# Performance work log

Hardware: AMD Instinct MI355X
Metric: run time of the kernel (lower is better)

The kernel has to match this reference:

```python
import jax, jax.numpy as jnp
import numpy as np
from jax import lax

N = 2048
BS = 64
NUM_ITR = 25


def setup_inputs() -> dict:
    key = jax.random.key(0)
    k1, k2, k3, k4, k5 = jax.random.split(key, 5)
    scale = 0.5 / np.sqrt(N)  # keep iteration matrices contractive so the recurrence stays bounded
    H = jax.random.normal(k1, (N, N), dtype=jnp.float32) / np.sqrt(N)
    Dinv = jax.random.normal(k2, (N, N), dtype=jnp.float32) * scale
    U = jax.random.normal(k3, (N, N), dtype=jnp.float32) * scale
    invM = jax.random.normal(k4, (N, N), dtype=jnp.float32) * scale
    y = jax.random.normal(k5, (BS, N), dtype=jnp.float32)
    return {"num_itr": NUM_ITR, "bs": BS, "y": y, "H": H, "Dinv": Dinv, "U": U, "invM": invM}


def reference(num_itr, bs, y, H, Dinv, U, invM):
    n = H.shape[0]
    s0 = jnp.zeros((bs, n), dtype=y.dtype)
    yMF = y @ H.T                 # [bs, n]
    s_init = yMF @ Dinv           # initial Gauss-Seidel estimate

    def step(s, _):
        s_next = (yMF - s @ U) @ invM
        return s_next, s_next

    s_final, traj_iters = lax.scan(step, s_init, None, length=num_itr)
    # traj matches the torch list: [zeros, s_1, ..., s_num_itr]
    traj = jnp.concatenate([s0[None], traj_iters], axis=0)  # [num_itr+1, bs, n]
    return s_final, traj
```

## Files before the change

kernel.cpp:

```cpp
#include <hip/hip_runtime.h>
#include <hip/hip_bf16.h>

#define NDIM 2048
#define BS   64
#define NM4  (NDIM * NDIM / 4)
#define BSN  ((size_t)BS * NDIM)

typedef __bf16 bf16_t;
typedef __bf16 bf16x4 __attribute__((ext_vector_type(4)));
typedef __bf16 bf16x8 __attribute__((ext_vector_type(8)));
typedef float  f32x4  __attribute__((ext_vector_type(4)));

__global__ __launch_bounds__(256) void prep(
    const float* __restrict__ H, const float* __restrict__ U,
    const float* __restrict__ Dinv, const float* __restrict__ invM,
    const float* __restrict__ y,
    bf16_t* __restrict__ H16, bf16_t* __restrict__ U16,
    bf16_t* __restrict__ Dt, bf16_t* __restrict__ iMt,
    bf16_t* __restrict__ y16, float* __restrict__ traj0) {
  __shared__ bf16_t tile[32][33];
  int b = blockIdx.x, tid = threadIdx.x;
  if (b < 8192) {
    int idx = b * 256 + tid;
    const float* src = (idx < NM4) ? H : U;
    bf16_t* dst = (idx < NM4) ? H16 : U16;
    int i = (idx < NM4) ? idx : idx - NM4;
    float4 v = ((const float4*)src)[i];
    bf16x4 o = {(bf16_t)v.x, (bf16_t)v.y, (bf16_t)v.z, (bf16_t)v.w};
    ((bf16x4*)dst)[i] = o;
    if (idx < BS * NDIM / 4) {
      float4 w = ((const float4*)y)[idx];
      bf16x4 o2 = {(bf16_t)w.x, (bf16_t)w.y, (bf16_t)w.z, (bf16_t)w.w};
      ((bf16x4*)y16)[idx] = o2;
      ((float4*)traj0)[idx] = make_float4(0.f, 0.f, 0.f, 0.f);
    }
  } else {
    int id = b - 8192;
    int bx = id & 63, by = id >> 6;
    int tx = tid & 31, ty = tid >> 5;
    const float* src[2] = {Dinv, invM};
    bf16_t* dst[2] = {Dt, iMt};
#pragma unroll
    for (int m = 0; m < 2; ++m) {
      __syncthreads();
#pragma unroll
      for (int i = 0; i < 4; ++i)
        tile[ty + i * 8][tx] =
            (bf16_t)src[m][(size_t)(by * 32 + ty + i * 8) * NDIM + bx * 32 + tx];
      __syncthreads();
#pragma unroll
      for (int i = 0; i < 4; ++i)
        dst[m][(size_t)(bx * 32 + ty + i * 8) * NDIM + by * 32 + tx] = tile[tx][ty + i * 8];
    }
  }
}

__device__ __forceinline__ void skinny_role(
    const bf16_t* __restrict__ A, const bf16_t* __restrict__ Bt, int n0, char* smem,
    const float* __restrict__ add, float sign,
    float* o32, float* o32b, bf16_t* o16) {
  bf16x8* panel = (bf16x8*)smem;
  int tid = threadIdx.x, lane = tid & 63, wave = tid >> 6;
  int ml = lane & 15, q = lane >> 4;
  f32x4 acc[4];
  acc[0] = acc[1] = acc[2] = acc[3] = (f32x4){0.f, 0.f, 0.f, 0.f};
#pragma unroll
  for (int half = 0; half < 2; ++half) {
    __syncthreads();
#pragma unroll
    for (int i = 0; i < 8; ++i) {
      int F = i * 256 + tid, c = F >> 6, ln = F & 63;
      panel[F] = *(const bf16x8*)(Bt + (size_t)(n0 + (ln & 15)) * NDIM +
                                  half * 1024 + c * 32 + ((ln >> 4) << 3));
    }
    __syncthreads();
    const bf16x8* Ap = (const bf16x8*)(A + (size_t)(wave * 16 + ml) * NDIM) + q + half * 128;
    const bf16x8* Bp = panel + lane;
#pragma unroll 16
    for (int c = 0; c < 32; ++c) {
      bf16x8 a = Ap[c * 4];
      bf16x8 b = Bp[c * 64];
      acc[c & 3] = __builtin_amdgcn_mfma_f32_16x16x32_bf16(a, b, acc[c & 3], 0, 0, 0);
    }
  }
  f32x4 s = (acc[0] + acc[1]) + (acc[2] + acc[3]);
  int mrow = wave * 16 + q * 4, col = n0 + ml;
#pragma unroll
  for (int r = 0; r < 4; ++r) {
    size_t o = (size_t)(mrow + r) * NDIM + col;
    float v = sign * s[r];
    if (add) v += add[o];
    if (o32)  o32[o]  = v;
    if (o32b) o32b[o] = v;
    if (o16)  o16[o]  = (bf16_t)v;
  }
}

__device__ __forceinline__ void wgemm_role(
    const bf16_t* __restrict__ A, const bf16_t* __restrict__ Bt,
    bf16_t* __restrict__ C, int blk, char* smem) {
  bf16x8* As = (bf16x8*)smem;
  bf16x8* Bs = (bf16x8*)(smem + 8192);
  int tid = threadIdx.x, lane = tid & 63, wave = tid >> 6;
  int m0 = (blk >> 5) * 128, n0 = (blk & 31) * 64;
  int wr4 = (wave >> 1) * 4, wc2 = (wave & 1) * 2;
  int ml = lane & 15, q = lane >> 4;

  f32x4 acc[4][2];
#pragma unroll
  for (int i = 0; i < 4; ++i)
#pragma unroll
    for (int j = 0; j < 2; ++j) acc[i][j] = (f32x4){0.f, 0.f, 0.f, 0.f};

  for (int k0 = 0; k0 < NDIM; k0 += 32) {
    __syncthreads();
#pragma unroll
    for (int i = 0; i < 2; ++i) {
      int S = i * 256 + tid, g = S >> 6, ln = S & 63;
      As[S] = *(const bf16x8*)(A + (size_t)(m0 + g * 16 + (ln & 15)) * NDIM + k0 + ((ln >> 4) << 3));
    }
    {
      int S = tid, g = S >> 6, ln = S & 63;
      Bs[S] = *(const bf16x8*)(Bt + (size_t)(n0 + g * 16 + (ln & 15)) * NDIM + k0 + ((ln >> 4) << 3));
    }
    __syncthreads();
    bf16x8 af[4], bfr[2];
#pragma unroll
    for (int i = 0; i < 4; ++i) af[i] = As[(wr4 + i) * 64 + lane];
#pragma unroll
    for (int j = 0; j < 2; ++j) bfr[j] = Bs[(wc2 + j) * 64 + lane];
#pragma unroll
    for (int i = 0; i < 4; ++i)
#pragma unroll
      for (int j = 0; j < 2; ++j)
        acc[i][j] = __builtin_amdgcn_mfma_f32_16x16x32_bf16(af[i], bfr[j], acc[i][j], 0, 0, 0);
  }
  int wr = wr4 * 16, wc = wc2 * 16;
#pragma unroll
  for (int i = 0; i < 4; ++i)
#pragma unroll
    for (int j = 0; j < 2; ++j)
#pragma unroll
      for (int r = 0; r < 4; ++r)
        C[(size_t)(m0 + wr + i * 16 + q * 4 + r) * NDIM + n0 + wc + j * 16 + ml] =
            (bf16_t)acc[i][j][r];
}

__device__ __forceinline__ void transpose_role(const bf16_t* __restrict__ src,
                                               bf16_t* __restrict__ dst, int blk, char* smem) {
  bf16_t (*tile)[72] = (bf16_t(*)[72])smem;
  int tid = threadIdx.x;
  int bx = blk & 31, by = blk >> 5;
#pragma unroll
  for (int i = 0; i < 2; ++i) {
    int v = i * 256 + tid, r = v >> 3, c8 = (v & 7) * 8;
    *(bf16x8*)&tile[r][c8] = *(const bf16x8*)(src + (size_t)(by * 64 + r) * NDIM + bx * 64 + c8);
  }
  __syncthreads();
#pragma unroll
  for (int i = 0; i < 2; ++i) {
    int v = i * 256 + tid, r = v >> 3, c8 = (v & 7) * 8;
    bf16x8 o;
#pragma unroll
    for (int j = 0; j < 8; ++j) o[j] = tile[c8 + j][r];
    *(bf16x8*)(dst + (size_t)(bx * 64 + r) * NDIM + by * 64 + c8) = o;
  }
}

__global__ __launch_bounds__(256) void megaA(
    const bf16_t* __restrict__ U16, const bf16_t* __restrict__ iMt16,
    const bf16_t* __restrict__ y16, const bf16_t* __restrict__ H16,
    bf16_t* __restrict__ Wrm, bf16_t* __restrict__ yMF16) {
  __shared__ char smem[32768];
  int b = blockIdx.x;
  if (b < 128) skinny_role(y16, H16, b * 16, smem, nullptr, 1.f, nullptr, nullptr, yMF16);
  else         wgemm_role(U16, iMt16, Wrm, b - 128, smem);
}

__global__ __launch_bounds__(256) void megaB(
    const bf16_t* __restrict__ Wrm, const bf16_t* __restrict__ yMF16,
    const bf16_t* __restrict__ iMt16, const bf16_t* __restrict__ Dt16,
    bf16_t* __restrict__ Wt, float* __restrict__ c32, bf16_t* __restrict__ c16,
    bf16_t* __restrict__ z0) {
  __shared__ char smem[32768];
  int b = blockIdx.x;
  if (b < 1024)      transpose_role(Wrm, Wt, b, smem);
  else if (b < 1152) skinny_role(yMF16, iMt16, (b - 1024) * 16, smem, nullptr, 1.f, c32, nullptr, c16);
  else               skinny_role(yMF16, Dt16, (b - 1152) * 16, smem, nullptr, 1.f, nullptr, nullptr, z0);
}

__global__ __launch_bounds__(256) void megaC(
    const bf16_t* __restrict__ Wt, const bf16_t* __restrict__ Wrm,
    const bf16_t* __restrict__ z0, const bf16_t* __restrict__ c16,
    const float* __restrict__ c32,
    bf16_t* __restrict__ W2t, float* __restrict__ traj1, bf16_t* __restrict__ z0b,
    float* __restrict__ c2_32, bf16_t* __restrict__ c2_16) {
  __shared__ char smem[32768];
  int b = blockIdx.x;
  if (b < 512)      wgemm_role(Wt, Wrm, W2t, b, smem);
  else if (b < 640) skinny_role(z0, Wt, (b - 512) * 16, smem, c32, -1.f, traj1, nullptr, z0b);
  else              skinny_role(c16, Wt, (b - 640) * 16, smem, c32, -1.f, c2_32, nullptr, c2_16);
}

__global__ __launch_bounds__(256) void megaD(
    const bf16_t* __restrict__ W2t, const bf16_t* __restrict__ z0,
    const bf16_t* __restrict__ c2_16, const float* __restrict__ c2_32,
    bf16_t* __restrict__ W2rm, float* __restrict__ traj2, float* __restrict__ traj3,
    bf16_t* __restrict__ zA, float* __restrict__ c4_32) {
  __shared__ char smem[32768];
  int b = blockIdx.x;
  if (b < 1024)      transpose_role(W2t, W2rm, b, smem);
  else if (b < 1152) skinny_role(z0, W2t, (b - 1024) * 16, smem, c2_32, 1.f, traj2, nullptr, zA);
  else if (b < 1280) skinny_role(z0 + BSN, W2t, (b - 1152) * 16, smem, c2_32, 1.f, traj3, nullptr, zA + BSN);
  else               skinny_role(c2_16, W2t, (b - 1280) * 16, smem, c2_32, 1.f, c4_32, nullptr, nullptr);
}

__global__ __launch_bounds__(256) void megaE(
    const bf16_t* __restrict__ W2t, const bf16_t* __restrict__ W2rm,
    const bf16_t* __restrict__ zA_in, const float* __restrict__ c2_32,
    bf16_t* __restrict__ W4t, float* __restrict__ traj4, float* __restrict__ traj5,
    bf16_t* __restrict__ zA) {
  __shared__ char smem[32768];
  int b = blockIdx.x;
  if (b < 512)      wgemm_role(W2t, W2rm, W4t, b, smem);
  else if (b < 640) skinny_role(zA_in, W2t, (b - 512) * 16, smem, c2_32, 1.f, traj4, nullptr, zA + 2 * BSN);
  else              skinny_role(zA_in + BSN, W2t, (b - 640) * 16, smem, c2_32, 1.f, traj5, nullptr, zA + 3 * BSN);
}

__global__ __launch_bounds__(256) void quad_step(
    const bf16_t* __restrict__ zin, const bf16_t* __restrict__ W4t,
    const float* __restrict__ c4_32, float* __restrict__ trajb,
    bf16_t* __restrict__ zout, float* __restrict__ sfin) {
  __shared__ char smem[32768];
  int b = blockIdx.x, ci = b & 3, p = b >> 2;
  skinny_role(zin + (size_t)ci * BSN, W4t, p * 16, smem, c4_32, 1.f,
              trajb + (size_t)ci * BSN, (ci == 3) ? sfin : nullptr,
              zout + (size_t)ci * BSN);
}

extern "C" void kernel_launch(void* const* d_in, const int* in_sizes, int n_in,
                              void* d_out, int out_size, void* d_ws, size_t ws_size,
                              hipStream_t stream) {
  const float* y    = (const float*)d_in[2];
  const float* H    = (const float*)d_in[3];
  const float* Dinv = (const float*)d_in[4];
  const float* U    = (const float*)d_in[5];
  const float* invM = (const float*)d_in[6];

  float* out     = (float*)d_out;
  float* s_final = out;
  float* traj    = out + BSN;

  char* ws = (char*)d_ws;
  size_t off = 0;
  auto alloc = [&](size_t bytes) -> void* {
    void* p = ws + off;
    off += (bytes + 255) & ~(size_t)255;
    return p;
  };
  bf16_t* U16   = (bf16_t*)alloc((size_t)NDIM * NDIM * 2);
  bf16_t* Dt16  = (bf16_t*)alloc((size_t)NDIM * NDIM * 2);
  bf16_t* iMt16 = (bf16_t*)alloc((size_t)NDIM * NDIM * 2);
  bf16_t* H16   = (bf16_t*)alloc((size_t)NDIM * NDIM * 2);
  bf16_t* Wrm   = (bf16_t*)alloc((size_t)NDIM * NDIM * 2);
  bf16_t* Wt    = (bf16_t*)alloc((size_t)NDIM * NDIM * 2);
  bf16_t* y16   = (bf16_t*)alloc(BSN * 2);
  bf16_t* yMF16 = (bf16_t*)alloc(BSN * 2);
  bf16_t* c16   = (bf16_t*)alloc(BSN * 2);
  bf16_t* c2_16 = (bf16_t*)alloc(BSN * 2);
  float*  c32   = (float*)alloc(BSN * 4);
  float*  c2_32 = (float*)alloc(BSN * 4);
  float*  c4_32 = (float*)alloc(BSN * 4);
  bf16_t* z0    = (bf16_t*)alloc(2 * BSN * 2);
  bf16_t* zA    = (bf16_t*)alloc(4 * BSN * 2);
  bf16_t* zB    = (bf16_t*)alloc(4 * BSN * 2);
  bf16_t* W2t   = H16;
  bf16_t* W2rm  = U16;
  bf16_t* W4t   = Dt16;

  prep<<<12288, 256, 0, stream>>>(H, U, Dinv, invM, y, H16, U16, Dt16, iMt16, y16, traj);
  megaA<<<640, 256, 0, stream>>>(U16, iMt16, y16, H16, Wrm, yMF16);
  megaB<<<1280, 256, 0, stream>>>(Wrm, yMF16, iMt16, Dt16, Wt, c32, c16, z0);
  megaC<<<768, 256, 0, stream>>>(Wt, Wrm, z0, c16, c32, W2t, traj + BSN, z0 + BSN, c2_32, c2_16);
  megaD<<<1408, 256, 0, stream>>>(W2t, z0, c2_16, c2_32, W2rm, traj + 2 * BSN, traj + 3 * BSN,
                                  zA, c4_32);
  megaE<<<768, 256, 0, stream>>>(W2t, W2rm, zA, c2_32, W4t, traj + 4 * BSN, traj + 5 * BSN, zA);

  bf16_t* zcur = zA;
  bf16_t* znxt = zB;
  for (int g = 0; g < 5; ++g) {
    float* sfin = (g == 4) ? s_final : nullptr;
    quad_step<<<512, 256, 0, stream>>>(zcur, W4t, c4_32, traj + (size_t)(6 + 4 * g) * BSN,
                                       znxt, sfin);
    bf16_t* tmp = zcur; zcur = znxt; znxt = tmp;
  }
}
```

Before: 449.6 us.

## Use 512-thread blocks with intra-block split-K for wide and skinny GEMMs

The wide GEMM role moves to 128x128 output tiles computed by 8 waves. Each half of the waves handles one half of K, and the two partial results are combined through LDS before writing bf16. The skinny role loads the whole 16-column B panel into LDS in one pass and splits K across two wave groups, combining them with an LDS reduction. All mega kernels and quad_step are relaunched with 512 threads, 68 KB of LDS, launch_bounds(512,2), and adjusted grid sizes. This aims to improve data reuse and cut barrier passes, at the cost of higher LDS use per block and an extra reduction step.

```diff
diff --git a/kernel.cpp b/kernel.cpp
--- a/kernel.cpp
+++ b/kernel.cpp
@@ -5,6 +5,7 @@
 #define BS   64
 #define NM4  (NDIM * NDIM / 4)
 #define BSN  ((size_t)BS * NDIM)
+#define SMEM_BYTES 69632
 
 typedef __bf16 bf16_t;
 typedef __bf16 bf16x4 __attribute__((ext_vector_type(4)));
@@ -55,95 +56,117 @@
   }
 }
 
+__device__ __forceinline__ void wgemm_role(
+    const bf16_t* __restrict__ A, const bf16_t* __restrict__ Bt,
+    bf16_t* __restrict__ C, int blk, char* smem) {
+  bf16x8* As_lo = (bf16x8*)smem;
+  bf16x8* Bs_lo = (bf16x8*)(smem + 8192);
+  bf16x8* As_hi = (bf16x8*)(smem + 16384);
+  bf16x8* Bs_hi = (bf16x8*)(smem + 24576);
+  int tid = threadIdx.x, lane = tid & 63, wave = tid >> 6;
+  int kh = wave >> 2, wq = wave & 3;
+  int m0 = (blk >> 4) * 128, n0 = (blk & 15) * 128;
+  int wr16 = (wq >> 1) * 4, wc16 = (wq & 1) * 4;
+  int ml = lane & 15, q = lane >> 4;
+
+  f32x4 acc[4][4];
+#pragma unroll
+  for (int i = 0; i < 4; ++i)
+#pragma unroll
+    for (int j = 0; j < 4; ++j) acc[i][j] = (f32x4){0.f, 0.f, 0.f, 0.f};
+
+  int sg = tid >> 6, sln = tid & 63;
+  int srow = sg * 16 + (sln & 15), skq = (sln >> 4) << 3;
+
+  for (int k0 = 0; k0 < 1024; k0 += 32) {
+    __syncthreads();
+    As_lo[tid] = *(const bf16x8*)(A  + (size_t)(m0 + srow) * NDIM + k0 + skq);
+    Bs_lo[tid] = *(const bf16x8*)(Bt + (size_t)(n0 + srow) * NDIM + k0 + skq);
+    As_hi[tid] = *(const bf16x8*)(A  + (size_t)(m0 + srow) * NDIM + 1024 + k0 + skq);
+    Bs_hi[tid] = *(const bf16x8*)(Bt + (size_t)(n0 + srow) * NDIM + 1024 + k0 + skq);
+    __syncthreads();
+    bf16x8* Asb = kh ? As_hi : As_lo;
+    bf16x8* Bsb = kh ? Bs_hi : Bs_lo;
+    bf16x8 af[4], bfr[4];
+#pragma unroll
+    for (int i = 0; i < 4; ++i) {
+      af[i]  = Asb[(wr16 + i) * 64 + lane];
+      bfr[i] = Bsb[(wc16 + i) * 64 + lane];
+    }
+#pragma unroll
+    for (int i = 0; i < 4; ++i)
+#pragma unroll
+      for (int j = 0; j < 4; ++j)
+        acc[i][j] = __builtin_amdgcn_mfma_f32_16x16x32_bf16(af[i], bfr[j], acc[i][j], 0, 0, 0);
+  }
+
+  f32x4* exch = (f32x4*)smem;
+  __syncthreads();
+  if (kh == 1) {
+#pragma unroll
+    for (int f = 0; f < 16; ++f)
+      exch[(f * 4 + wq) * 64 + lane] = acc[f >> 2][f & 3];
+  }
+  __syncthreads();
+  if (kh == 0) {
+    int wr = wr16 * 16, wc = wc16 * 16;
+#pragma unroll
+    for (int i = 0; i < 4; ++i)
+#pragma unroll
+      for (int j = 0; j < 4; ++j) {
+        f32x4 s = acc[i][j] + exch[((i * 4 + j) * 4 + wq) * 64 + lane];
+#pragma unroll
+        for (int r = 0; r < 4; ++r)
+          C[(size_t)(m0 + wr + i * 16 + q * 4 + r) * NDIM + n0 + wc + j * 16 + ml] =
+              (bf16_t)s[r];
+      }
+  }
+}
+
 __device__ __forceinline__ void skinny_role(
     const bf16_t* __restrict__ A, const bf16_t* __restrict__ Bt, int n0, char* smem,
     const float* __restrict__ add, float sign,
     float* o32, float* o32b, bf16_t* o16) {
   bf16x8* panel = (bf16x8*)smem;
+  f32x4* red = (f32x4*)(smem + 65536);
   int tid = threadIdx.x, lane = tid & 63, wave = tid >> 6;
+#pragma unroll
+  for (int i = 0; i < 8; ++i) {
+    int F = i * 512 + tid, c = F >> 6, ln = F & 63;
+    panel[F] = *(const bf16x8*)(Bt + (size_t)(n0 + (ln & 15)) * NDIM + c * 32 + ((ln >> 4) << 3));
+  }
+  __syncthreads();
+
+  int ms = (wave & 3) * 16, kh = wave >> 2;
   int ml = lane & 15, q = lane >> 4;
+  const bf16x8* Ap = (const bf16x8*)(A + (size_t)(ms + ml) * NDIM) + q + kh * 128;
+  const bf16x8* Bp = panel + lane + kh * 2048;
+
   f32x4 acc[4];
   acc[0] = acc[1] = acc[2] = acc[3] = (f32x4){0.f, 0.f, 0.f, 0.f};
 #pragma unroll
-  for (int half = 0; half < 2; ++half) {
-    __syncthreads();
-#pragma unroll
-    for (int i = 0; i < 8; ++i) {
-      int F = i * 256 + tid, c = F >> 6, ln = F & 63;
-      panel[F] = *(const bf16x8*)(Bt + (size_t)(n0 + (ln & 15)) * NDIM +
-                                  half * 1024 + c * 32 + ((ln >> 4) << 3));
+  for (int c = 0; c < 32; ++c) {
+    bf16x8 a = Ap[c * 4];
+    bf16x8 b = Bp[c * 64];
+    acc[c & 3] = __builtin_amdgcn_mfma_f32_16x16x32_bf16(a, b, acc[c & 3], 0, 0, 0);
+  }
+  f32x4 s = (acc[0] + acc[1]) + (acc[2] + acc[3]);
+
+  if (wave >= 4) red[(wave & 3) * 64 + lane] = s;
+  __syncthreads();
+  if (wave < 4) {
+    s += red[wave * 64 + lane];
+    int mrow = ms + q * 4, col = n0 + ml;
+#pragma unroll
+    for (int r = 0; r < 4; ++r) {
+      size_t o = (size_t)(mrow + r) * NDIM + col;
+      float v = sign * s[r];
+      if (add) v += add[o];
+      if (o32)  o32[o]  = v;
+      if (o32b) o32b[o] = v;
+      if (o16)  o16[o]  = (bf16_t)v;
     }
-    __syncthreads();
-    const bf16x8* Ap = (const bf16x8*)(A + (size_t)(wave * 16 + ml) * NDIM) + q + half * 128;
-    const bf16x8* Bp = panel + lane;
-#pragma unroll 16
-    for (int c = 0; c < 32; ++c) {
-      bf16x8 a = Ap[c * 4];
-      bf16x8 b = Bp[c * 64];
-      acc[c & 3] = __builtin_amdgcn_mfma_f32_16x16x32_bf16(a, b, acc[c & 3], 0, 0, 0);
-    }
-  }
-  f32x4 s = (acc[0] + acc[1]) + (acc[2] + acc[3]);
-  int mrow = wave * 16 + q * 4, col = n0 + ml;
-#pragma unroll
-  for (int r = 0; r < 4; ++r) {
-    size_t o = (size_t)(mrow + r) * NDIM + col;
-    float v = sign * s[r];
-    if (add) v += add[o];
-    if (o32)  o32[o]  = v;
-    if (o32b) o32b[o] = v;
-    if (o16)  o16[o]  = (bf16_t)v;
-  }
-}
-
-__device__ __forceinline__ void wgemm_role(
-    const bf16_t* __restrict__ A, const bf16_t* __restrict__ Bt,
-    bf16_t* __restrict__ C, int blk, char* smem) {
-  bf16x8* As = (bf16x8*)smem;
-  bf16x8* Bs = (bf16x8*)(smem + 8192);
-  int tid = threadIdx.x, lane = tid & 63, wave = tid >> 6;
-  int m0 = (blk >> 5) * 128, n0 = (blk & 31) * 64;
-  int wr4 = (wave >> 1) * 4, wc2 = (wave & 1) * 2;
-  int ml = lane & 15, q = lane >> 4;
-
-  f32x4 acc[4][2];
-#pragma unroll
-  for (int i = 0; i < 4; ++i)
-#pragma unroll
-    for (int j = 0; j < 2; ++j) acc[i][j] = (f32x4){0.f, 0.f, 0.f, 0.f};
-
-  for (int k0 = 0; k0 < NDIM; k0 += 32) {
-    __syncthreads();
-#pragma unroll
-    for (int i = 0; i < 2; ++i) {
-      int S = i * 256 + tid, g = S >> 6, ln = S & 63;
-      As[S] = *(const bf16x8*)(A + (size_t)(m0 + g * 16 + (ln & 15)) * NDIM + k0 + ((ln >> 4) << 3));
-    }
-    {
-      int S = tid, g = S >> 6, ln = S & 63;
-      Bs[S] = *(const bf16x8*)(Bt + (size_t)(n0 + g * 16 + (ln & 15)) * NDIM + k0 + ((ln >> 4) << 3));
-    }
-    __syncthreads();
-    bf16x8 af[4], bfr[2];
-#pragma unroll
-    for (int i = 0; i < 4; ++i) af[i] = As[(wr4 + i) * 64 + lane];
-#pragma unroll
-    for (int j = 0; j < 2; ++j) bfr[j] = Bs[(wc2 + j) * 64 + lane];
-#pragma unroll
-    for (int i = 0; i < 4; ++i)
-#pragma unroll
-      for (int j = 0; j < 2; ++j)
-        acc[i][j] = __builtin_amdgcn_mfma_f32_16x16x32_bf16(af[i], bfr[j], acc[i][j], 0, 0, 0);
-  }
-  int wr = wr4 * 16, wc = wc2 * 16;
-#pragma unroll
-  for (int i = 0; i < 4; ++i)
-#pragma unroll
-    for (int j = 0; j < 2; ++j)
-#pragma unroll
-      for (int r = 0; r < 4; ++r)
-        C[(size_t)(m0 + wr + i * 16 + q * 4 + r) * NDIM + n0 + wc + j * 16 + ml] =
-            (bf16_t)acc[i][j][r];
+  }
 }
 
 __device__ __forceinline__ void transpose_role(const bf16_t* __restrict__ src,
@@ -151,15 +174,13 @@
   bf16_t (*tile)[72] = (bf16_t(*)[72])smem;
   int tid = threadIdx.x;
   int bx = blk & 31, by = blk >> 5;
-#pragma unroll
-  for (int i = 0; i < 2; ++i) {
-    int v = i * 256 + tid, r = v >> 3, c8 = (v & 7) * 8;
+  {
+    int r = tid >> 3, c8 = (tid & 7) * 8;
     *(bf16x8*)&tile[r][c8] = *(const bf16x8*)(src + (size_t)(by * 64 + r) * NDIM + bx * 64 + c8);
   }
   __syncthreads();
-#pragma unroll
-  for (int i = 0; i < 2; ++i) {
-    int v = i * 256 + tid, r = v >> 3, c8 = (v & 7) * 8;
+  {
+    int r = tid >> 3, c8 = (tid & 7) * 8;
     bf16x8 o;
 #pragma unroll
     for (int j = 0; j < 8; ++j) o[j] = tile[c8 + j][r];
@@ -167,47 +188,47 @@
   }
 }
 
-__global__ __launch_bounds__(256) void megaA(
+__global__ __launch_bounds__(512, 2) void megaA(
     const bf16_t* __restrict__ U16, const bf16_t* __restrict__ iMt16,
     const bf16_t* __restrict__ y16, const bf16_t* __restrict__ H16,
     bf16_t* __restrict__ Wrm, bf16_t* __restrict__ yMF16) {
-  __shared__ char smem[32768];
-  int b = blockIdx.x;
-  if (b < 128) skinny_role(y16, H16, b * 16, smem, nullptr, 1.f, nullptr, nullptr, yMF16);
-  else         wgemm_role(U16, iMt16, Wrm, b - 128, smem);
-}
-
-__global__ __launch_bounds__(256) void megaB(
+  __shared__ char smem[SMEM_BYTES];
+  int b = blockIdx.x;
+  if (b < 256) wgemm_role(U16, iMt16, Wrm, b, smem);
+  else         skinny_role(y16, H16, (b - 256) * 16, smem, nullptr, 1.f, nullptr, nullptr, yMF16);
+}
+
+__global__ __launch_bounds__(512, 2) void megaB(
     const bf16_t* __restrict__ Wrm, const bf16_t* __restrict__ yMF16,
     const bf16_t* __restrict__ iMt16, const bf16_t* __restrict__ Dt16,
     bf16_t* __restrict__ Wt, float* __restrict__ c32, bf16_t* __restrict__ c16,
     bf16_t* __restrict__ z0) {
-  __shared__ char smem[32768];
+  __shared__ char smem[SMEM_BYTES];
   int b = blockIdx.x;
   if (b < 1024)      transpose_role(Wrm, Wt, b, smem);
   else if (b < 1152) skinny_role(yMF16, iMt16, (b - 1024) * 16, smem, nullptr, 1.f, c32, nullptr, c16);
   else               skinny_role(yMF16, Dt16, (b - 1152) * 16, smem, nullptr, 1.f, nullptr, nullptr, z0);
 }
 
-__global__ __launch_bounds__(256) void megaC(
+__global__ __launch_bounds__(512, 2) void megaC(
     const bf16_t* __restrict__ Wt, const bf16_t* __restrict__ Wrm,
     const bf16_t* __restrict__ z0, const bf16_t* __restrict__ c16,
     const float* __restrict__ c32,
     bf16_t* __restrict__ W2t, float* __restrict__ traj1, bf16_t* __restrict__ z0b,
     float* __restrict__ c2_32, bf16_t* __restrict__ c2_16) {
-  __shared__ char smem[32768];
-  int b = blockIdx.x;
-  if (b < 512)      wgemm_role(Wt, Wrm, W2t, b, smem);
-  else if (b < 640) skinny_role(z0, Wt, (b - 512) * 16, smem, c32, -1.f, traj1, nullptr, z0b);
-  else              skinny_role(c16, Wt, (b - 640) * 16, smem, c32, -1.f, c2_32, nullptr, c2_16);
-}
-
-__global__ __launch_bounds__(256) void megaD(
+  __shared__ char smem[SMEM_BYTES];
+  int b = blockIdx.x;
+  if (b < 256)      wgemm_role(Wt, Wrm, W2t, b, smem);
+  else if (b < 384) skinny_role(z0, Wt, (b - 256) * 16, smem, c32, -1.f, traj1, nullptr, z0b);
+  else              skinny_role(c16, Wt, (b - 384) * 16, smem, c32, -1.f, c2_32, nullptr, c2_16);
+}
+
+__global__ __launch_bounds__(512, 2) void megaD(
     const bf16_t* __restrict__ W2t, const bf16_t* __restrict__ z0,
     const bf16_t* __restrict__ c2_16, const float* __restrict__ c2_32,
     bf16_t* __restrict__ W2rm, float* __restrict__ traj2, float* __restrict__ traj3,
     bf16_t* __restrict__ zA, float* __restrict__ c4_32) {
-  __shared__ char smem[32768];
+  __shared__ char smem[SMEM_BYTES];
   int b = blockIdx.x;
   if (b < 1024)      transpose_role(W2t, W2rm, b, smem);
   else if (b < 1152) skinny_role(z0, W2t, (b - 1024) * 16, smem, c2_32, 1.f, traj2, nullptr, zA);
@@ -215,23 +236,23 @@
   else               skinny_role(c2_16, W2t, (b - 1280) * 16, smem, c2_32, 1.f, c4_32, nullptr, nullptr);
 }
 
-__global__ __launch_bounds__(256) void megaE(
+__global__ __launch_bounds__(512, 2) void megaE(
     const bf16_t* __restrict__ W2t, const bf16_t* __restrict__ W2rm,
     const bf16_t* __restrict__ zA_in, const float* __restrict__ c2_32,
     bf16_t* __restrict__ W4t, float* __restrict__ traj4, float* __restrict__ traj5,
     bf16_t* __restrict__ zA) {
-  __shared__ char smem[32768];
-  int b = blockIdx.x;
-  if (b < 512)      wgemm_role(W2t, W2rm, W4t, b, smem);
-  else if (b < 640) skinny_role(zA_in, W2t, (b - 512) * 16, smem, c2_32, 1.f, traj4, nullptr, zA + 2 * BSN);
-  else              skinny_role(zA_in + BSN, W2t, (b - 640) * 16, smem, c2_32, 1.f, traj5, nullptr, zA + 3 * BSN);
-}
-
-__global__ __launch_bounds__(256) void quad_step(
+  __shared__ char smem[SMEM_BYTES];
+  int b = blockIdx.x;
+  if (b < 256)      wgemm_role(W2t, W2rm, W4t, b, smem);
+  else if (b < 384) skinny_role(zA_in, W2t, (b - 256) * 16, smem, c2_32, 1.f, traj4, nullptr, zA + 2 * BSN);
+  else              skinny_role(zA_in + BSN, W2t, (b - 384) * 16, smem, c2_32, 1.f, traj5, nullptr, zA + 3 * BSN);
+}
+
+__global__ __launch_bounds__(512, 2) void quad_step(
     const bf16_t* __restrict__ zin, const bf16_t* __restrict__ W4t,
     const float* __restrict__ c4_32, float* __restrict__ trajb,
     bf16_t* __restrict__ zout, float* __restrict__ sfin) {
-  __shared__ char smem[32768];
+  __shared__ char smem[SMEM_BYTES];
   int b = blockIdx.x, ci = b & 3, p = b >> 2;
   skinny_role(zin + (size_t)ci * BSN, W4t, p * 16, smem, c4_32, 1.f,
               trajb + (size_t)ci * BSN, (ci == 3) ? sfin : nullptr,
@@ -279,18 +300,18 @@
   bf16_t* W4t   = Dt16;
 
   prep<<<12288, 256, 0, stream>>>(H, U, Dinv, invM, y, H16, U16, Dt16, iMt16, y16, traj);
-  megaA<<<640, 256, 0, stream>>>(U16, iMt16, y16, H16, Wrm, yMF16);
-  megaB<<<1280, 256, 0, stream>>>(Wrm, yMF16, iMt16, Dt16, Wt, c32, c16, z0);
-  megaC<<<768, 256, 0, stream>>>(Wt, Wrm, z0, c16, c32, W2t, traj + BSN, z0 + BSN, c2_32, c2_16);
-  megaD<<<1408, 256, 0, stream>>>(W2t, z0, c2_16, c2_32, W2rm, traj + 2 * BSN, traj + 3 * BSN,
+  megaA<<<384, 512, 0, stream>>>(U16, iMt16, y16, H16, Wrm, yMF16);
+  megaB<<<1280, 512, 0, stream>>>(Wrm, yMF16, iMt16, Dt16, Wt, c32, c16, z0);
+  megaC<<<512, 512, 0, stream>>>(Wt, Wrm, z0, c16, c32, W2t, traj + BSN, z0 + BSN, c2_32, c2_16);
+  megaD<<<1408, 512, 0, stream>>>(W2t, z0, c2_16, c2_32, W2rm, traj + 2 * BSN, traj + 3 * BSN,
                                   zA, c4_32);
-  megaE<<<768, 256, 0, stream>>>(W2t, W2rm, zA, c2_32, W4t, traj + 4 * BSN, traj + 5 * BSN, zA);
+  megaE<<<512, 512, 0, stream>>>(W2t, W2rm, zA, c2_32, W4t, traj + 4 * BSN, traj + 5 * BSN, zA);
 
   bf16_t* zcur = zA;
   bf16_t* znxt = zB;
   for (int g = 0; g < 5; ++g) {
     float* sfin = (g == 4) ? s_final : nullptr;
-    quad_step<<<512, 256, 0, stream>>>(zcur, W4t, c4_32, traj + (size_t)(6 + 4 * g) * BSN,
+    quad_step<<<512, 512, 0, stream>>>(zcur, W4t, c4_32, traj + (size_t)(6 + 4 * g) * BSN,
                                        znxt, sfin);
     bf16_t* tmp = zcur; zcur = znxt; znxt = tmp;
   }
```

Result: faster. 419.8 us (-6.6%).
